# Performance work log

Hardware: AMD Instinct MI355X
Metric: run time of the kernel (lower is better)

## Reference

```python
import jax, jax.numpy as jnp
import numpy as np

KH = KW = 3
SH = SW = 1
PH = PW = 1


def _im2col(x, kh, kw, sh, sw, ph, pw):
    # x: [N, C, H, W] -> cols: [N, C*kh*kw, H_out*W_out], ordering (C, kh, kw)
    N, C, H, W = x.shape
    H_out = (H + 2 * ph - kh) // sh + 1
    W_out = (W + 2 * pw - kw) // sw + 1
    x_pad = jnp.pad(x, ((0, 0), (0, 0), (ph, ph), (pw, pw)))
    # fixed small loop over kernel offsets (kh*kw = 9), strided slices
    patches = [x_pad[:, :, i:i + sh * H_out:sh, j:j + sw * W_out:sw]
               for i in range(kh) for j in range(kw)]  # each [N, C, H_out, W_out]
    cols = jnp.stack(patches, axis=2)  # [N, C, kh*kw, H_out, W_out]
    cols = cols.reshape(N, C * kh * kw, H_out * W_out)
    return cols, H_out, W_out


def setup_inputs() -> dict:
    key = jax.random.key(0)
    k1, k2, k3 = jax.random.split(key, 3)
    x = jax.random.normal(k1, (16, 128, 56, 56), dtype=jnp.float32)
    weight = jax.random.normal(k2, (256, 128, 3, 3), dtype=jnp.float32) * 0.05
    fan_in = 128 * 3 * 3
    bound = 1.0 / fan_in ** 0.5
    bias = jax.random.uniform(k3, (256,), dtype=jnp.float32, minval=-bound, maxval=bound)
    return {"x": x, "weight": weight, "bias": bias}


def reference(x, weight, bias):
    # im2col unfold + (analog) matmul conv; noise_cfg=None -> plain matmul
    cols, H_out, W_out = _im2col(x, KH, KW, SH, SW, PH, PW)  # [N, K, L]
    N = cols.shape[0]
    Cout = weight.shape[0]
    Wmat = weight.reshape(Cout, -1)  # [Cout, K], K = C*kh*kw
    # y[n, l, o] = sum_k cols[n, k, l] * Wmat[o, k]  (AnalogMatMulFn without noise)
    y = jnp.einsum('nkl,ok->nol', cols, Wmat)  # [N, Cout, L]
    y = y.reshape(N, Cout, H_out, W_out)
    y = y + bias[None, :, None, None]
    return y
```

## Files before the change

kernel.cpp:

```cpp
#include <hip/hip_runtime.h>
#include <hip/hip_bf16.h>
#include <stdint.h>


typedef __attribute__((ext_vector_type(8))) short short8;
typedef __attribute__((ext_vector_type(4))) float floatx4;

__device__ static inline void gload_lds16(const void* g, void* l) {
  typedef const __attribute__((address_space(1))) unsigned int* gp_t;
  typedef __attribute__((address_space(3))) unsigned int* lp_t;
  __builtin_amdgcn_global_load_lds((gp_t)(uintptr_t)g, (lp_t)(uint32_t)(uintptr_t)l,
                                   16, 0, 0);
}

__global__ __launch_bounds__(256)
void xpose_kernel(const float* __restrict__ x, __hip_bfloat16* __restrict__ xp) {
  const int n = blockIdx.x / 56;
  const int h = blockIdx.x % 56;
  __shared__ float tile[128][57];
  const float* src = x + (size_t)n * (128 * 3136) + h * 56;
  for (int idx = threadIdx.x; idx < 128 * 56; idx += 256) {
    const int c = idx / 56, w = idx - c * 56;
    tile[c][w] = src[(size_t)c * 3136 + w];
  }
  __syncthreads();
  __hip_bfloat16* dst = xp + ((size_t)(n * 58 + h + 1) * 58 + 1) * 128;
  for (int idx = threadIdx.x; idx < 56 * 64; idx += 256) {
    const int w = idx >> 6, c2 = idx & 63;
    union { unsigned u; __hip_bfloat16 h2[2]; } pk;
    pk.h2[0] = __float2bfloat16(tile[2 * c2][w]);
    pk.h2[1] = __float2bfloat16(tile[2 * c2 + 1][w]);
    *(unsigned*)(dst + (size_t)w * 128 + 2 * c2) = pk.u;
  }
}

__global__ __launch_bounds__(256)
void wxf_kernel(const float* __restrict__ wsrc, __hip_bfloat16* __restrict__ wt) {
  const int t = blockIdx.x * 256 + threadIdx.x;
  if (t >= 256 * 9 * 128) return;
  const int c = t & 127;
  const int kq = (t >> 7) % 9;
  const int cout = t / (9 * 128);
  wt[t] = __float2bfloat16(wsrc[(size_t)(cout * 128 + c) * 9 + kq]);
}

__global__ __launch_bounds__(256)
void conv_gemm_kernel(const __hip_bfloat16* __restrict__ xp,
                      const __hip_bfloat16* __restrict__ wt,
                      const float* __restrict__ bias,
                      float* __restrict__ out) {
  __shared__ __align__(16) __hip_bfloat16 As[128 * 64];
  __shared__ __align__(16) __hip_bfloat16 Bs[128 * 64];

  const int tid = threadIdx.x;
  const int lane = tid & 63;
  const int wave = tid >> 6;
  const int wm = wave >> 1, wn = wave & 1;
  const int m0 = blockIdx.y * 128;
  const int n0 = blockIdx.x * 128;

  const char* wtb = (const char*)wt;
  const char* xpb = (const char*)xp;
  const char* gA[4];
  const char* gB[4];
  char* lA[4];
  char* lB[4];
#pragma unroll
  for (int i = 0; i < 4; ++i) {
    const int f = (i * 256 + tid) * 16;
    const int row = f >> 7;
    const int sub = (f >> 4) & 7;
    const int cb = (sub ^ (row & 7)) << 4;
    gA[i] = wtb + (size_t)(m0 + row) * 2304 + cb;
    const int pix = n0 + row;
    const int nimg = pix / 3136;
    const int rem = pix - nimg * 3136;
    const int hh = rem / 56;
    const int ww = rem - hh * 56;
    gB[i] = xpb + (size_t)((nimg * 58 + hh) * 58 + ww) * 256 + cb;
    lA[i] = (char*)As + i * 4096 + wave * 1024;
    lB[i] = (char*)Bs + i * 4096 + wave * 1024;
  }

  const int quad = lane >> 4;
  const int x7 = lane & 7;
  const int arow = (wm * 64 + (lane & 15)) * 128;
  const int brow = (wn * 64 + (lane & 15)) * 128;
  int cko[2];
  cko[0] = ((0 + quad) ^ x7) << 4;
  cko[1] = ((4 + quad) ^ x7) << 4;

  floatx4 acc[4][4];
#pragma unroll
  for (int a = 0; a < 4; ++a)
#pragma unroll
    for (int b = 0; b < 4; ++b) acc[a][b] = (floatx4)0.f;

#pragma unroll 1
  for (int kq = 0; kq < 9; ++kq) {
    const int kh = kq / 3;
    const int kw_ = kq - kh * 3;
    const int btap = (kh * 58 + kw_) * 256;
#pragma unroll 1
    for (int ch = 0; ch < 2; ++ch) {
      const int aofs = kq * 256 + ch * 128;
      const int bofs = btap + ch * 128;
      __syncthreads();
#pragma unroll
      for (int i = 0; i < 4; ++i) {
        gload_lds16(gA[i] + aofs, lA[i]);
        gload_lds16(gB[i] + bofs, lB[i]);
      }
      __syncthreads();
#pragma unroll
      for (int ks = 0; ks < 2; ++ks) {
        short8 af[4], bf[4];
#pragma unroll
        for (int mt = 0; mt < 4; ++mt)
          af[mt] = *(const short8*)((const char*)As + arow + mt * (16 * 128) + cko[ks]);
#pragma unroll
        for (int nt = 0; nt < 4; ++nt)
          bf[nt] = *(const short8*)((const char*)Bs + brow + nt * (16 * 128) + cko[ks]);
#pragma unroll
        for (int mt = 0; mt < 4; ++mt)
#pragma unroll
          for (int nt = 0; nt < 4; ++nt)
            acc[mt][nt] = __builtin_amdgcn_mfma_f32_16x16x32_bf16(
                af[mt], bf[nt], acc[mt][nt], 0, 0, 0);
      }
    }
  }

  const int col = lane & 15;
  const int rb = (lane >> 4) * 4;
#pragma unroll
  for (int nt = 0; nt < 4; ++nt) {
    const int pix = n0 + wn * 64 + nt * 16 + col;
    const int nimg = pix / 3136;
    const int rem = pix - nimg * 3136;
    float* op = out + (size_t)nimg * (256 * 3136) + rem;
#pragma unroll
    for (int mt = 0; mt < 4; ++mt) {
      const int mb = m0 + wm * 64 + mt * 16 + rb;
#pragma unroll
      for (int r = 0; r < 4; ++r) {
        op[(size_t)(mb + r) * 3136] = acc[mt][nt][r] + bias[mb + r];
      }
    }
  }
}

__global__ __launch_bounds__(256)
void direct_conv_kernel(const float* __restrict__ x, const float* __restrict__ wgt,
                        const float* __restrict__ bias, float* __restrict__ out) {
  const long t = (long)blockIdx.x * 256 + threadIdx.x;
  if (t >= 16L * 256 * 3136) return;
  const int w = t % 56;
  const int h = (t / 56) % 56;
  const int o = (t / 3136) % 256;
  const int n = t / (256L * 3136);
  float s = bias[o];
  for (int c = 0; c < 128; ++c)
    for (int kh = 0; kh < 3; ++kh) {
      const int hh = h + kh - 1;
      if (hh < 0 || hh >= 56) continue;
      for (int kw = 0; kw < 3; ++kw) {
        const int ww = w + kw - 1;
        if (ww < 0 || ww >= 56) continue;
        s += x[((size_t)(n * 128 + c) * 56 + hh) * 56 + ww] *
             wgt[((size_t)(o * 128 + c) * 3 + kh) * 3 + kw];
      }
    }
  out[t] = s;
}

extern "C" void kernel_launch(void* const* d_in, const int* in_sizes, int n_in,
                              void* d_out, int out_size, void* d_ws, size_t ws_size,
                              hipStream_t stream) {
  const float* x = (const float*)d_in[0];
  const float* w = (const float*)d_in[1];
  const float* b = (const float*)d_in[2];
  float* out = (float*)d_out;

  const size_t xp_bytes = (size_t)16 * 58 * 58 * 128 * 2;
  const size_t wt_bytes = (size_t)256 * 9 * 128 * 2;

  if (ws_size >= xp_bytes + wt_bytes) {
    __hip_bfloat16* xp = (__hip_bfloat16*)d_ws;
    __hip_bfloat16* wt = (__hip_bfloat16*)((char*)d_ws + xp_bytes);
    (void)hipMemsetAsync(d_ws, 0, xp_bytes, stream);
    hipLaunchKernelGGL(xpose_kernel, dim3(16 * 56), dim3(256), 0, stream, x, xp);
    hipLaunchKernelGGL(wxf_kernel, dim3(1152), dim3(256), 0, stream, w, wt);
    hipLaunchKernelGGL(conv_gemm_kernel, dim3(392, 2), dim3(256), 0, stream,
                       xp, wt, b, out);
  } else {
    const long total = 16L * 256 * 3136;
    hipLaunchKernelGGL(direct_conv_kernel, dim3((unsigned)((total + 255) / 256)),
                       dim3(256), 0, stream, x, w, b, out);
  }
}
```

Baseline: 142.9 us.

## Fuse pad/transpose/weight prep into one kernel and remap GEMM blocks per XCD

Merges the padding memset, input transpose to bf16 NHWC, and the weight reorder into a single pre-kernel that writes the zero border itself and uses vectorized float4 loads and 16-byte stores. This removes a full memset pass over the padded buffer and two extra launches. The GEMM grid is flattened and remapped so that blocks landing on the same XCD work on a contiguous range of pixel tiles, with the aim of better L2 reuse of activations. The weight conversion now runs in only 36 blocks, which could lengthen the prep stage.

```diff
diff --git a/kernel.cpp b/kernel.cpp
--- a/kernel.cpp
+++ b/kernel.cpp
@@ -14,34 +14,52 @@
 }
 
 __global__ __launch_bounds__(256)
-void xpose_kernel(const float* __restrict__ x, __hip_bfloat16* __restrict__ xp) {
-  const int n = blockIdx.x / 56;
-  const int h = blockIdx.x % 56;
-  __shared__ float tile[128][57];
-  const float* src = x + (size_t)n * (128 * 3136) + h * 56;
-  for (int idx = threadIdx.x; idx < 128 * 56; idx += 256) {
-    const int c = idx / 56, w = idx - c * 56;
-    tile[c][w] = src[(size_t)c * 3136 + w];
-  }
-  __syncthreads();
-  __hip_bfloat16* dst = xp + ((size_t)(n * 58 + h + 1) * 58 + 1) * 128;
-  for (int idx = threadIdx.x; idx < 56 * 64; idx += 256) {
-    const int w = idx >> 6, c2 = idx & 63;
-    union { unsigned u; __hip_bfloat16 h2[2]; } pk;
-    pk.h2[0] = __float2bfloat16(tile[2 * c2][w]);
-    pk.h2[1] = __float2bfloat16(tile[2 * c2 + 1][w]);
-    *(unsigned*)(dst + (size_t)w * 128 + 2 * c2) = pk.u;
-  }
-}
-
-__global__ __launch_bounds__(256)
-void wxf_kernel(const float* __restrict__ wsrc, __hip_bfloat16* __restrict__ wt) {
-  const int t = blockIdx.x * 256 + threadIdx.x;
-  if (t >= 256 * 9 * 128) return;
-  const int c = t & 127;
-  const int kq = (t >> 7) % 9;
-  const int cout = t / (9 * 128);
-  wt[t] = __float2bfloat16(wsrc[(size_t)(cout * 128 + c) * 9 + kq]);
+void pre_kernel(const float* __restrict__ x, const float* __restrict__ wsrc,
+                __hip_bfloat16* __restrict__ xp, __hip_bfloat16* __restrict__ wt) {
+  const int b = blockIdx.x;
+  if (b < 16 * 58) {
+    const int n = b / 58, hp = b % 58;
+    __hip_bfloat16* dst = xp + (size_t)(n * 58 + hp) * 58 * 128;
+    if (hp == 0 || hp == 57) {
+      const uint4 z = {0, 0, 0, 0};
+      uint4* p = (uint4*)dst;
+      for (int i = threadIdx.x; i < 928; i += 256) p[i] = z;
+      return;
+    }
+    const int h = hp - 1;
+    __shared__ float tile[128][57];
+    const float* src = x + (size_t)n * (128 * 3136) + h * 56;
+    for (int i = threadIdx.x; i < 128 * 14; i += 256) {
+      const int c = i / 14, q = i - c * 14;
+      const float4 v = ((const float4*)(src + (size_t)c * 3136))[q];
+      tile[c][4 * q + 0] = v.x;
+      tile[c][4 * q + 1] = v.y;
+      tile[c][4 * q + 2] = v.z;
+      tile[c][4 * q + 3] = v.w;
+    }
+    __syncthreads();
+    if (threadIdx.x < 32) {
+      const uint4 z = {0, 0, 0, 0};
+      const int col = (threadIdx.x >> 4) * 57;
+      ((uint4*)(dst + (size_t)col * 128))[threadIdx.x & 15] = z;
+    }
+    __hip_bfloat16* di = dst + 128;
+    for (int i = threadIdx.x; i < 56 * 16; i += 256) {
+      const int w = i >> 4, c8 = (i & 15) * 8;
+      union { uint4 u; __hip_bfloat16 hh[8]; } pk;
+#pragma unroll
+      for (int j = 0; j < 8; ++j) pk.hh[j] = __float2bfloat16(tile[c8 + j][w]);
+      *(uint4*)(di + (size_t)w * 128 + c8) = pk.u;
+    }
+  } else {
+    const int base = (b - 928) * 256 + threadIdx.x;
+    for (int t = base; t < 256 * 9 * 128; t += 36 * 256) {
+      const int c = t & 127;
+      const int kq = (t >> 7) % 9;
+      const int cout = t / (9 * 128);
+      wt[t] = __float2bfloat16(wsrc[(size_t)(cout * 128 + c) * 9 + kq]);
+    }
+  }
 }
 
 __global__ __launch_bounds__(256)
@@ -56,8 +74,14 @@
   const int lane = tid & 63;
   const int wave = tid >> 6;
   const int wm = wave >> 1, wn = wave & 1;
-  const int m0 = blockIdx.y * 128;
-  const int n0 = blockIdx.x * 128;
+
+  const int id = blockIdx.x;
+  const int xcd = id & 7;
+  const int r = id >> 3;
+  const int mt_ = r / 49;
+  const int nt_ = xcd * 49 + (r - mt_ * 49);
+  const int m0 = mt_ * 128;
+  const int n0 = nt_ * 128;
 
   const char* wtb = (const char*)wt;
   const char* xpb = (const char*)xp;
@@ -94,7 +118,7 @@
 #pragma unroll
   for (int a = 0; a < 4; ++a)
 #pragma unroll
-    for (int b = 0; b < 4; ++b) acc[a][b] = (floatx4)0.f;
+    for (int c = 0; c < 4; ++c) acc[a][c] = (floatx4)0.f;
 
 #pragma unroll 1
   for (int kq = 0; kq < 9; ++kq) {
@@ -143,8 +167,8 @@
     for (int mt = 0; mt < 4; ++mt) {
       const int mb = m0 + wm * 64 + mt * 16 + rb;
 #pragma unroll
-      for (int r = 0; r < 4; ++r) {
-        op[(size_t)(mb + r) * 3136] = acc[mt][nt][r] + bias[mb + r];
+      for (int rr = 0; rr < 4; ++rr) {
+        op[(size_t)(mb + rr) * 3136] = acc[mt][nt][rr] + bias[mb + rr];
       }
     }
   }
@@ -188,10 +212,9 @@
   if (ws_size >= xp_bytes + wt_bytes) {
     __hip_bfloat16* xp = (__hip_bfloat16*)d_ws;
     __hip_bfloat16* wt = (__hip_bfloat16*)((char*)d_ws + xp_bytes);
-    (void)hipMemsetAsync(d_ws, 0, xp_bytes, stream);
-    hipLaunchKernelGGL(xpose_kernel, dim3(16 * 56), dim3(256), 0, stream, x, xp);
-    hipLaunchKernelGGL(wxf_kernel, dim3(1152), dim3(256), 0, stream, w, wt);
-    hipLaunchKernelGGL(conv_gemm_kernel, dim3(392, 2), dim3(256), 0, stream,
+    hipLaunchKernelGGL(pre_kernel, dim3(16 * 58 + 36), dim3(256), 0, stream,
+                       x, w, xp, wt);
+    hipLaunchKernelGGL(conv_gemm_kernel, dim3(784), dim3(256), 0, stream,
                        xp, wt, b, out);
   } else {
     const long total = 16L * 256 * 3136;
```

Measured after the change: 138.2 us. -3.3%, faster.
